# Optimization experiments

Hardware: AMD Instinct MI355X
Metric: run time of the kernel (lower is better)

## Reference

```python
import jax, jax.numpy as jnp
import numpy as np

B, S, D, P, H = 32, 1024, 512, 720, 4   # batch, seq_len (=codebook_size), enc_in, pred_len, heads
COMMIT_W, ORTHO_W = 1.0, 0.8


def setup_inputs() -> dict:
    key = jax.random.key(0)
    ks = jax.random.split(key, 6)
    return {
        "x": jax.random.normal(ks[0], (B, S, D), jnp.float32),
        "w_in": jax.random.normal(ks[1], (H * D, D), jnp.float32) * 0.02,   # project_in: dim -> heads*dim
        "b_in": jnp.zeros((H * D,), jnp.float32),
        "embed": jax.random.normal(ks[2], (H, S, D), jnp.float32),          # per-head codebook [h, C, d]
        "w_out": jax.random.normal(ks[3], (D, H * D), jnp.float32) * 0.02,  # project_out: heads*dim -> dim
        "b_out": jnp.zeros((D,), jnp.float32),
        "w_lin": jax.random.normal(ks[4], (P, S), jnp.float32) * 0.02,      # Linear over time axis
        "b_lin": jnp.zeros((P,), jnp.float32),
    }


def reference(x, w_in, b_in, embed, w_out, b_out, w_lin, b_lin):
    C = embed.shape[1]
    # Normalization: subtract last timestep (detached)
    seq_last = jax.lax.stop_gradient(x[:, -1:, :])          # [B,1,D]
    x0 = x - seq_last                                       # [B,S,D]

    # --- VectorQuantize ---
    xi = x0 @ w_in.T + b_in                                 # [B,S,H*D] project_in
    # 'b n (h d) -> h (b n) d' (separate codebook per head)
    f = xi.reshape(B, S, H, D).transpose(2, 0, 1, 3).reshape(H, B * S, D)
    # squared-euclidean distances to codes: [H, B*S, C]
    d2 = (jnp.sum(f * f, -1, keepdims=True)
          - 2.0 * jnp.einsum('hnd,hcd->hnc', f, embed)
          + jnp.sum(embed * embed, -1)[:, None, :])
    ind = jnp.argmin(d2, axis=-1)                           # [H, B*S]
    q = jnp.take_along_axis(embed, ind[:, :, None], axis=1)  # gather -> [H, B*S, D]

    # commitment loss (learnable codebook => quantize NOT detached)
    commit_loss = jnp.mean((q - f) ** 2)
    # orthogonal regularization on full codebook
    normed = embed / jnp.linalg.norm(embed, axis=-1, keepdims=True)
    cs = jnp.einsum('hid,hjd->hij', normed, normed)         # [H,C,C]
    ortho_loss = jnp.sum(cs ** 2) / (H * C * C) - 1.0 / C
    loss = COMMIT_W * commit_loss + ORTHO_W * ortho_loss

    # straight-through estimator
    q_st = f + jax.lax.stop_gradient(q - f)
    # 'h (b n) d -> b n (h d)'
    qo = q_st.reshape(H, B, S, D).transpose(1, 2, 0, 3).reshape(B, S, H * D)
    quantized = qo @ w_out.T + b_out                        # [B,S,D] project_out

    # Linear over the time axis: permute(0,2,1) -> Linear(S->P) -> permute back
    y = jnp.einsum('bnd,pn->bpd', quantized, w_lin) + b_lin[None, :, None]
    y = y + seq_last                                        # [B,P,D]

    indices = ind.reshape(H, B, S).transpose(1, 2, 0)       # [B,S,H]
    return y, indices, loss
```

## Files before the change

kernel.cpp:

```cpp
#include <hip/hip_runtime.h>
#include <stdint.h>

typedef unsigned int u32;
typedef unsigned long long u64;
typedef _Float16 f16;
typedef __attribute__((ext_vector_type(8))) _Float16 f16x8;
typedef __attribute__((ext_vector_type(4))) _Float16 f16x4;
typedef __attribute__((ext_vector_type(2))) _Float16 f16x2;
typedef __attribute__((ext_vector_type(4))) float f32x4;

#define MFMA16(a, b, c) __builtin_amdgcn_mfma_f32_16x16x32_f16((a), (b), (c), 0, 0, 0)
#define MARGIN 2.0f
#define WAITV(n) asm volatile("s_waitcnt vmcnt(" #n ")" ::: "memory")

__device__ __forceinline__ u32 ford(float x) { u32 u = __float_as_uint(x); return (u & 0x80000000u) ? ~u : (u | 0x80000000u); }
__device__ __forceinline__ float iford(u32 v) { u32 u = (v & 0x80000000u) ? (v & 0x7FFFFFFFu) : ~v; return __uint_as_float(u); }
__device__ __forceinline__ int xswz(int i, int n) { return (i & 7) * (n >> 3) + (i >> 3); }

typedef __attribute__((address_space(1))) const unsigned char ga_t;
typedef __attribute__((address_space(3))) unsigned char la_t;
__device__ __forceinline__ void gl16(const void* g, void* l) {
  __builtin_amdgcn_global_load_lds((ga_t*)g, (la_t*)l, 16, 0, 0);
}

__device__ __forceinline__ void stgp(const f16* g, int kt, char* sdst, int tid) {
#pragma unroll
  for (int it = 0; it < 2; ++it) {
    const int u = (tid + (it << 9)) << 4;
    const int r = u >> 7, sl = (u >> 4) & 7;
    const char* src = (const char*)g + (size_t)r * 1024 + ((size_t)kt << 7) +
                      (size_t)((sl ^ (r & 7)) << 4);
    gl16(src, sdst + u);
  }
}

__device__ __forceinline__ f16x8 rdf(const char* bb, int pb, int rr, int ks, int lane) {
  return *(const f16x8*)(bb + pb + rr * 128 +
                         ((((ks << 2) + (lane >> 4)) ^ (rr & 7)) << 4));
}

template <bool ISK1>
__global__ __launch_bounds__(512, 1) void gemm8(
    const f16* __restrict__ A0, const f16* __restrict__ A1,
    const f16* __restrict__ B0, const f16* __restrict__ B1,
    int chrows, void* __restrict__ out0, void* __restrict__ out1,
    const float* __restrict__ bias, const float* __restrict__ aux) {
  __shared__ char lds[131072 + (ISK1 ? 0 : 4096)];
  const int tid = threadIdx.x;
  const int lane = tid & 63, wid = tid >> 6;
  const int wm = wid >> 2, wn = wid & 3;

  int blkm, blkn, z = 0;
  {
    const int s = xswz(blockIdx.x, gridDim.x);
    if constexpr (ISK1) { blkn = s & 15; blkm = s >> 4; }
    else {
      const int bph = (chrows >> 8) << 2;
      z = s / bph;
      const int rem = s - z * bph;
      blkm = rem >> 2; blkn = rem & 3;
    }
  }

  if constexpr (!ISK1) {
    ((int*)(lds + 131072))[tid] = 0;
    ((int*)(lds + 131072))[tid + 512] = 0;
  }

  const f16 *p0, *p1, *p2, *p3;
  if constexpr (ISK1) {
    p0 = A0 + (size_t)blkm * 65536;
    p1 = A1 + (size_t)blkm * 65536;
    p2 = B0 + (size_t)blkn * 65536;
    p3 = B1 + (size_t)blkn * 65536;
  } else {
    p0 = A0 + ((size_t)z * chrows + (size_t)blkm * 256) * 512;
    p1 = p0 + 65536;
    p2 = B0 + (size_t)z * 524288 + (size_t)blkn * 131072;
    p3 = p2 + 65536;
  }

  constexpr int NACC = ISK1 ? 8 : 32;
  f32x4 acc[NACC];
#pragma unroll
  for (int i = 0; i < NACC; ++i) acc[i] = f32x4{0.f, 0.f, 0.f, 0.f};

  stgp(p0, 0, lds + 0, tid);
  stgp(p1, 0, lds + 16384, tid);
  stgp(p2, 0, lds + 32768, tid);
  stgp(p3, 0, lds + 49152, tid);

#pragma unroll
  for (int kc = 0; kc < 8; ++kc) {
    const char* bb = lds + (kc & 1) * 65536;
    char* nb = lds + ((kc + 1) & 1) * 65536;
    const bool pf = (kc + 1 < 8);
    WAITV(0);
    __builtin_amdgcn_s_barrier();

    if constexpr (!ISK1) {
      f16x8 a[4][2], b[4][2];
      const int pbA = wm * 16384;
      const int pbB = 32768 + (wn >> 1) * 16384;
      const int rB = (wn & 1) * 64 + (lane & 15);
#pragma unroll
      for (int mt = 0; mt < 4; ++mt)
#pragma unroll
        for (int ks = 0; ks < 2; ++ks) a[mt][ks] = rdf(bb, pbA, mt * 16 + (lane & 15), ks, lane);
#pragma unroll
      for (int nt = 0; nt < 2; ++nt)
#pragma unroll
        for (int ks = 0; ks < 2; ++ks) b[nt][ks] = rdf(bb, pbB, rB + nt * 16, ks, lane);
      if (pf) stgp(p0, kc + 1, nb + 0, tid);
      __builtin_amdgcn_s_setprio(1);
#pragma unroll
      for (int nt = 0; nt < 2; ++nt)
#pragma unroll
        for (int mt = 0; mt < 4; ++mt)
#pragma unroll
          for (int ks = 0; ks < 2; ++ks) acc[mt * 4 + nt] = MFMA16(a[mt][ks], b[nt][ks], acc[mt * 4 + nt]);
      __builtin_amdgcn_s_setprio(0);
#pragma unroll
      for (int nt = 2; nt < 4; ++nt)
#pragma unroll
        for (int ks = 0; ks < 2; ++ks) b[nt][ks] = rdf(bb, pbB, rB + nt * 16, ks, lane);
      if (pf) stgp(p1, kc + 1, nb + 16384, tid);
      __builtin_amdgcn_s_setprio(1);
#pragma unroll
      for (int nt = 2; nt < 4; ++nt)
#pragma unroll
        for (int mt = 0; mt < 4; ++mt)
#pragma unroll
          for (int ks = 0; ks < 2; ++ks) acc[mt * 4 + nt] = MFMA16(a[mt][ks], b[nt][ks], acc[mt * 4 + nt]);
      __builtin_amdgcn_s_setprio(0);
#pragma unroll
      for (int mt = 0; mt < 4; ++mt)
#pragma unroll
        for (int ks = 0; ks < 2; ++ks) a[mt][ks] = rdf(bb, pbA, (mt + 4) * 16 + (lane & 15), ks, lane);
      if (pf) stgp(p2, kc + 1, nb + 32768, tid);
      __builtin_amdgcn_s_setprio(1);
#pragma unroll
      for (int nt = 2; nt < 4; ++nt)
#pragma unroll
        for (int mt = 0; mt < 4; ++mt)
#pragma unroll
          for (int ks = 0; ks < 2; ++ks) acc[(mt + 4) * 4 + nt] = MFMA16(a[mt][ks], b[nt][ks], acc[(mt + 4) * 4 + nt]);
      __builtin_amdgcn_s_setprio(0);
      if (pf) stgp(p3, kc + 1, nb + 49152, tid);
      __builtin_amdgcn_s_setprio(1);
#pragma unroll
      for (int nt = 0; nt < 2; ++nt)
#pragma unroll
        for (int mt = 0; mt < 4; ++mt)
#pragma unroll
          for (int ks = 0; ks < 2; ++ks) acc[(mt + 4) * 4 + nt] = MFMA16(a[mt][ks], b[nt][ks], acc[(mt + 4) * 4 + nt]);
      __builtin_amdgcn_s_setprio(0);
    } else {
      f16x8 ah[2][2], al[2][2], bh[2][2], bl[2][2];
      const int rA = wm * 64 + (lane & 15);
      const int rB = wn * 32 + (lane & 15);
#pragma unroll
      for (int mt = 0; mt < 2; ++mt)
#pragma unroll
        for (int ks = 0; ks < 2; ++ks) {
          ah[mt][ks] = rdf(bb, 0, rA + mt * 16, ks, lane);
          al[mt][ks] = rdf(bb, 16384, rA + mt * 16, ks, lane);
        }
#pragma unroll
      for (int ks = 0; ks < 2; ++ks) {
        bh[0][ks] = rdf(bb, 32768, rB, ks, lane);
        bl[0][ks] = rdf(bb, 49152, rB, ks, lane);
      }
      if (pf) stgp(p0, kc + 1, nb + 0, tid);
      __builtin_amdgcn_s_setprio(1);
#pragma unroll
      for (int mt = 0; mt < 2; ++mt)
#pragma unroll
        for (int ks = 0; ks < 2; ++ks) {
          acc[mt * 2] = MFMA16(al[mt][ks], bh[0][ks], acc[mt * 2]);
          acc[mt * 2] = MFMA16(ah[mt][ks], bl[0][ks], acc[mt * 2]);
          acc[mt * 2] = MFMA16(ah[mt][ks], bh[0][ks], acc[mt * 2]);
        }
      __builtin_amdgcn_s_setprio(0);
#pragma unroll
      for (int ks = 0; ks < 2; ++ks) {
        bh[1][ks] = rdf(bb, 32768, rB + 16, ks, lane);
        bl[1][ks] = rdf(bb, 49152, rB + 16, ks, lane);
      }
      if (pf) stgp(p1, kc + 1, nb + 16384, tid);
      __builtin_amdgcn_s_setprio(1);
#pragma unroll
      for (int mt = 0; mt < 2; ++mt)
#pragma unroll
        for (int ks = 0; ks < 2; ++ks) {
          acc[mt * 2 + 1] = MFMA16(al[mt][ks], bh[1][ks], acc[mt * 2 + 1]);
          acc[mt * 2 + 1] = MFMA16(ah[mt][ks], bl[1][ks], acc[mt * 2 + 1]);
          acc[mt * 2 + 1] = MFMA16(ah[mt][ks], bh[1][ks], acc[mt * 2 + 1]);
        }
      __builtin_amdgcn_s_setprio(0);
#pragma unroll
      for (int mt = 0; mt < 2; ++mt)
#pragma unroll
        for (int ks = 0; ks < 2; ++ks) {
          ah[mt][ks] = rdf(bb, 0, rA + (mt + 2) * 16, ks, lane);
          al[mt][ks] = rdf(bb, 16384, rA + (mt + 2) * 16, ks, lane);
        }
      if (pf) stgp(p2, kc + 1, nb + 32768, tid);
      __builtin_amdgcn_s_setprio(1);
#pragma unroll
      for (int mt = 0; mt < 2; ++mt)
#pragma unroll
        for (int ks = 0; ks < 2; ++ks) {
          acc[(mt + 2) * 2 + 1] = MFMA16(al[mt][ks], bh[1][ks], acc[(mt + 2) * 2 + 1]);
          acc[(mt + 2) * 2 + 1] = MFMA16(ah[mt][ks], bl[1][ks], acc[(mt + 2) * 2 + 1]);
          acc[(mt + 2) * 2 + 1] = MFMA16(ah[mt][ks], bh[1][ks], acc[(mt + 2) * 2 + 1]);
        }
      __builtin_amdgcn_s_setprio(0);
      if (pf) stgp(p3, kc + 1, nb + 49152, tid);
      __builtin_amdgcn_s_setprio(1);
#pragma unroll
      for (int mt = 0; mt < 2; ++mt)
#pragma unroll
        for (int ks = 0; ks < 2; ++ks) {
          acc[(mt + 2) * 2] = MFMA16(al[mt][ks], bh[0][ks], acc[(mt + 2) * 2]);
          acc[(mt + 2) * 2] = MFMA16(ah[mt][ks], bl[0][ks], acc[(mt + 2) * 2]);
          acc[(mt + 2) * 2] = MFMA16(ah[mt][ks], bh[0][ks], acc[(mt + 2) * 2]);
        }
      __builtin_amdgcn_s_setprio(0);
    }
  }

  if constexpr (ISK1) {
    f16* fh = (f16*)out0;
    f16* fl = (f16*)out1;
#pragma unroll
    for (int nt = 0; nt < 2; ++nt) {
      const int gc = blkn * 128 + wn * 32 + nt * 16 + (lane & 15);
      const float bv = bias[gc];
      const int h = gc >> 9, d = gc & 511;
#pragma unroll
      for (int mt = 0; mt < 4; ++mt)
#pragma unroll
        for (int r = 0; r < 4; ++r) {
          const int grow = blkm * 128 + wm * 64 + mt * 16 + ((lane >> 4) << 2) + r;
          const float v = acc[mt * 2 + nt][r] * 6.103515625e-05f + bv;
          const f16 hv = (f16)v;
          const size_t off = ((size_t)h * chrows + grow) * 512 + d;
          fh[off] = hv;
          fl[off] = (f16)(v - (float)hv);
        }
    }
  } else {
    int* cntL = (int*)(lds + 131072);
    u64* candG = (u64*)out0;
    const int h = z;
    float escol[4];
    int cc[4];
#pragma unroll
    for (int nt = 0; nt < 4; ++nt) {
      cc[nt] = blkn * 256 + wn * 64 + nt * 16 + (lane & 15);
      escol[nt] = aux[h * 1024 + cc[nt]];
    }
#pragma unroll
    for (int mt = 0; mt < 8; ++mt)
#pragma unroll
      for (int r = 0; r < 4; ++r) {
        const int row_l = wm * 128 + mt * 16 + ((lane >> 4) << 2) + r;
        float vals[4];
        float mn = 3.4e38f;
#pragma unroll
        for (int nt = 0; nt < 4; ++nt) {
          const float v = escol[nt] - 2.0f * acc[mt * 4 + nt][r];
          vals[nt] = v;
          mn = fminf(mn, v);
        }
#pragma unroll
        for (int o = 1; o < 16; o <<= 1) mn = fminf(mn, __shfl_xor(mn, o));
        const float lim = mn + MARGIN;
#pragma unroll
        for (int nt = 0; nt < 4; ++nt)
          if (vals[nt] <= lim) {
            const int p = atomicAdd(&cntL[row_l * 4 + wn], 1);
            if (p < 4) {
              const size_t grow = (size_t)blkm * 256 + row_l;
              candG[((size_t)h * chrows + grow) * 64 + blkn * 16 + wn * 4 + p] =
                  ((u64)ford(vals[nt]) << 32) | (u32)cc[nt];
            }
          }
      }
  }
}

template <int LDK>
__device__ __forceinline__ void stg8k(const f16* gRowBase, int ktile, char* sdst, int tid) {
#pragma unroll
  for (int it = 0; it < 2; ++it) {
    const int u = (tid + (it << 8)) << 4;
    const int r = u >> 6, s = (u >> 4) & 3;
    const char* src = (const char*)gRowBase + (size_t)r * (LDK * 2) + ((size_t)ktile << 6) +
                      (size_t)((s ^ ((r >> 1) & 3)) << 4);
    gl16(src, sdst + u);
  }
}

template <int MODE>
__global__ __launch_bounds__(256, 3) void gemm2(
    const f16* __restrict__ Ah, const f16* __restrict__ Bh,
    void* __restrict__ out0, const float* __restrict__ bias,
    const float* __restrict__ aux, u64* __restrict__ slots) {
  constexpr int LDK = (MODE == 2 || MODE == 4) ? 1024 : 512;
  constexpr int D = 3;
  constexpr int KT = (MODE == 2 || MODE == 4) ? 32 : 16;
  constexpr int BUF = 16384;
  __shared__ char lds[D * BUF];

  const int tid = threadIdx.x;
  const int lane = tid & 63, wid = tid >> 6;
  const int wm = wid >> 1, wn = wid & 1;

  int blkm, blkn, z = 0;
  {
    const int s = xswz(blockIdx.x, gridDim.x);
    if constexpr (MODE == 1) { blkn = s & 3; blkm = s >> 2; z = blkm >> 3; }
    else if constexpr (MODE == 2) { blkn = s & 3; blkm = (s >> 2) & 3; z = s >> 4; }
    else { const int r2 = s % 24; blkm = r2 % 6; blkn = r2 / 6; z = s / 24; }
  }

  const f16 *Ab, *Bb;
  if constexpr (MODE == 1) {
    Ab = Ah + (size_t)blkm * 65536;
    Bb = Bh + (size_t)z * 262144 + (size_t)blkn * 65536;
  } else if constexpr (MODE == 2) {
    Ab = Ah + (size_t)z * 524288 + (size_t)blkm * 131072;
    Bb = Bh + (size_t)z * 524288 + (size_t)blkn * 131072;
  } else {
    Ab = Ah + (size_t)blkm * 131072;
    Bb = Bh + (size_t)z * 524288 + (size_t)blkn * 131072;
  }

  f32x4 acc[4][4];
#pragma unroll
  for (int i = 0; i < 4; ++i)
#pragma unroll
    for (int j = 0; j < 4; ++j) acc[i][j] = f32x4{0.f, 0.f, 0.f, 0.f};

  auto stage = [&](int kt, char* nb) {
    stg8k<LDK>(Ab, kt, nb, tid);
    stg8k<LDK>(Bb, kt, nb + 8192, tid);
  };
#pragma unroll
  for (int d = 0; d < D - 1; ++d) stage(d, lds + d * BUF);

#pragma unroll
  for (int kc = 0; kc < KT; ++kc) {
    if (kc + D - 1 < KT) stage(kc + D - 1, lds + ((kc + D - 1) % D) * BUF);
    const int nf = KT - 1 - kc;
    if (nf >= 2) WAITV(8);
    else if (nf == 1) WAITV(4);
    else WAITV(0);
    __builtin_amdgcn_s_barrier();
    const char* cbuf = lds + (kc % D) * BUF;
    f16x8 ah[4];
#pragma unroll
    for (int mt = 0; mt < 4; ++mt) {
      const int rr = wm * 64 + mt * 16 + (lane & 15);
      ah[mt] = *(const f16x8*)(cbuf + rr * 64 + (((lane >> 4) ^ ((rr >> 1) & 3)) << 4));
    }
    __builtin_amdgcn_s_setprio(1);
#pragma unroll
    for (int nt = 0; nt < 4; ++nt) {
      const int rn = wn * 64 + nt * 16 + (lane & 15);
      const f16x8 bh = *(const f16x8*)(cbuf + 8192 + rn * 64 + (((lane >> 4) ^ ((rn >> 1) & 3)) << 4));
#pragma unroll
      for (int mt = 0; mt < 4; ++mt) acc[mt][nt] = MFMA16(ah[mt], bh, acc[mt][nt]);
    }
    __builtin_amdgcn_s_setprio(0);
    __builtin_amdgcn_s_barrier();
  }

  if constexpr (MODE == 1) {
    f16* o = (f16*)out0;
#pragma unroll
    for (int nt = 0; nt < 4; ++nt) {
      const int gc = blkn * 128 + wn * 64 + nt * 16 + (lane & 15);
#pragma unroll
      for (int mt = 0; mt < 4; ++mt)
#pragma unroll
        for (int r = 0; r < 4; ++r) {
          const size_t grow = (size_t)blkm * 128 + wm * 64 + mt * 16 + ((lane >> 4) << 2) + r;
          o[grow * 512 + gc] = (f16)acc[mt][nt][r];
        }
    }
  } else if constexpr (MODE == 2) {
    float ssum = 0.f;
#pragma unroll
    for (int mt = 0; mt < 4; ++mt)
#pragma unroll
      for (int nt = 0; nt < 4; ++nt)
#pragma unroll
        for (int r = 0; r < 4; ++r) ssum += acc[mt][nt][r] * acc[mt][nt][r];
#pragma unroll
    for (int o = 1; o < 64; o <<= 1) ssum += __shfl_xor(ssum, o);
    float* wp = (float*)lds;
    __syncthreads();
    if (lane == 0) wp[wid] = ssum;
    __syncthreads();
    if (tid == 0) {
      const float p = wp[0] + wp[1] + wp[2] + wp[3];
      atomicAdd(slots + (blockIdx.x & 63), (u64)llrintf(p * 16777216.f));
    }
  } else {
    float* oy = (float*)out0 + (size_t)z * 368640;
    const float* xseq = aux + (size_t)z * 524288 + 523776;
    float sl[4];
    int gd[4];
#pragma unroll
    for (int nt = 0; nt < 4; ++nt) {
      gd[nt] = blkn * 128 + wn * 64 + nt * 16 + (lane & 15);
      sl[nt] = xseq[gd[nt]];
    }
#pragma unroll
    for (int mt = 0; mt < 4; ++mt)
#pragma unroll
      for (int r = 0; r < 4; ++r) {
        const int p = blkm * 128 + wm * 64 + mt * 16 + ((lane >> 4) << 2) + r;
        if (p < 720) {
          const float bp = bias[p];
#pragma unroll
          for (int nt = 0; nt < 4; ++nt) oy[(size_t)p * 512 + gd[nt]] = acc[mt][nt][r] + bp + sl[nt];
        }
      }
  }
}

__global__ __launch_bounds__(256, 4) void rescore_k(
    const u64* __restrict__ candG, const f16* __restrict__ fh,
    const f16* __restrict__ fl, const float* __restrict__ embed,
    int n0, int shCH,
    int* __restrict__ indw, float* __restrict__ indout, u64* __restrict__ cslots) {
  const int tid = threadIdx.x, lane = tid & 63, wid = tid >> 6;
  const int r = blockIdx.x * 4 + wid;
  const int h = r >> shCH, row = r & ((1 << shCH) - 1);
  u64 cu = candG[(size_t)r * 64 + lane];
  u64 mn = cu;
#pragma unroll
  for (int o = 1; o < 64; o <<= 1) { const u64 t = __shfl_xor(mn, o); if (t < mn) mn = t; }
  const float lim = iford((u32)(mn >> 32)) + MARGIN;
  const bool pass = iford((u32)(cu >> 32)) <= lim;
  u64 mask = __ballot(pass);
  float fv[8];
  {
    const size_t fo = (size_t)r * 512 + lane * 8;
    const f16x8 hv = *(const f16x8*)(fh + fo);
    const f16x8 lv = *(const f16x8*)(fl + fo);
#pragma unroll
    for (int j = 0; j < 8; ++j) fv[j] = (float)hv[j] + (float)lv[j];
  }
  double bestd = 1e300;
  int bestc = 0x7FFFFFFF;
  while (mask) {
    const int src = __ffsll((unsigned long long)mask) - 1;
    mask &= mask - 1;
    const int c = (int)(u32)__shfl(cu, src);
    const float* e = embed + ((size_t)h * 1024 + c) * 512 + lane * 8;
    const float4 e0 = *(const float4*)e, e1 = *(const float4*)(e + 4);
    const float ev[8] = {e0.x, e0.y, e0.z, e0.w, e1.x, e1.y, e1.z, e1.w};
    double sd = 0.0;
#pragma unroll
    for (int j = 0; j < 8; ++j) { const double d = (double)fv[j] - (double)ev[j]; sd += d * d; }
#pragma unroll
    for (int o = 1; o < 64; o <<= 1) sd += __shfl_xor(sd, o);
    if (sd < bestd || (sd == bestd && c < bestc)) { bestd = sd; bestc = c; }
  }
  if (lane == 0) {
    const int n = n0 + row;
    indw[(size_t)n * 4 + h] = bestc;
    indout[(size_t)n * 4 + h] = (float)bestc;
    atomicAdd(cslots + (blockIdx.x & 255), (u64)llrint(bestd * 65536.0));
  }
}

__global__ __launch_bounds__(256) void quantize_qT(
    const int* __restrict__ indw, const f16* __restrict__ Ep,
    const float* __restrict__ b_out, f16* __restrict__ qT) {
  const int tid = threadIdx.x;
  const int b = blockIdx.x >> 4, s0 = (blockIdx.x & 15) << 6;
  __shared__ int inds[64][4];
  inds[tid >> 2][tid & 3] = indw[(size_t)(b * 1024 + s0 + (tid >> 2)) * 4 + (tid & 3)];
  __syncthreads();
  const int d0 = tid * 2;
  const float ba0 = b_out[d0], ba1 = b_out[d0 + 1];
  u32 r0[32], r1[32];
  f16 t0 = (f16)0.f, t1 = (f16)0.f;
#pragma unroll
  for (int ss = 0; ss < 64; ++ss) {
    float a0 = ba0, a1 = ba1;
#pragma unroll
    for (int h = 0; h < 4; ++h) {
      const int c = inds[ss][h];
      const f16x2 p = *(const f16x2*)(Ep + (((size_t)h * 1024 + c) * 512 + d0));
      a0 += (float)p[0];
      a1 += (float)p[1];
    }
    const f16 q0 = (f16)a0, q1 = (f16)a1;
    if (ss & 1) {
      f16x2 w0; w0[0] = t0; w0[1] = q0; __builtin_memcpy(&r0[ss >> 1], &w0, 4);
      f16x2 w1; w1[0] = t1; w1[1] = q1; __builtin_memcpy(&r1[ss >> 1], &w1, 4);
    } else { t0 = q0; t1 = q1; }
  }
  const size_t o0 = ((size_t)b * 512 + d0) * 1024 + s0;
#pragma unroll
  for (int i = 0; i < 8; ++i) {
    uint4 v; v.x = r0[4 * i]; v.y = r0[4 * i + 1]; v.z = r0[4 * i + 2]; v.w = r0[4 * i + 3];
    *(uint4*)(qT + o0 + (size_t)i * 8) = v;
  }
  const size_t o1 = o0 + 1024;
#pragma unroll
  for (int i = 0; i < 8; ++i) {
    uint4 v; v.x = r1[4 * i]; v.y = r1[4 * i + 1]; v.z = r1[4 * i + 2]; v.w = r1[4 * i + 3];
    *(uint4*)(qT + o1 + (size_t)i * 8) = v;
  }
}

__global__ __launch_bounds__(256) void prep_x0(const float* __restrict__ x, int n0,
                                               f16* __restrict__ ht, f16* __restrict__ lt) {
  const int id = blockIdx.x * 256 + threadIdx.x;
  const int k8 = id & 63, r = id >> 6;
  const int n = n0 + r, b = n >> 10;
  const float* ap = x + (size_t)n * 512 + k8 * 8;
  const float* sp = x + (size_t)b * 524288 + 523776 + k8 * 8;
  const float4 a0 = *(const float4*)ap, a1 = *(const float4*)(ap + 4);
  const float4 s0 = *(const float4*)sp, s1 = *(const float4*)(sp + 4);
  const float v[8] = {(a0.x - s0.x) * 16.f, (a0.y - s0.y) * 16.f, (a0.z - s0.z) * 16.f,
                      (a0.w - s0.w) * 16.f, (a1.x - s1.x) * 16.f, (a1.y - s1.y) * 16.f,
                      (a1.z - s1.z) * 16.f, (a1.w - s1.w) * 16.f};
  f16x8 hv, lv;
#pragma unroll
  for (int j = 0; j < 8; ++j) { const f16 h = (f16)v[j]; hv[j] = h; lv[j] = (f16)(v[j] - (float)h); }
  const size_t off = (size_t)r * 512 + k8 * 8;
  *(f16x8*)(ht + off) = hv;
  *(f16x8*)(lt + off) = lv;
}

__global__ __launch_bounds__(256) void prep_win(const float* __restrict__ src,
                                                f16* __restrict__ hi, f16* __restrict__ lo) {
  const size_t e = ((size_t)blockIdx.x * 256 + threadIdx.x) * 4;
  const float4 v = *(const float4*)(src + e);
  const float w[4] = {v.x * 1024.f, v.y * 1024.f, v.z * 1024.f, v.w * 1024.f};
  f16x4 hv, lv;
#pragma unroll
  for (int j = 0; j < 4; ++j) { const f16 h = (f16)w[j]; hv[j] = h; lv[j] = (f16)(w[j] - (float)h); }
  *(f16x4*)(hi + e) = hv;
  *(f16x4*)(lo + e) = lv;
}

__global__ __launch_bounds__(256) void prep_embed_k(const float* __restrict__ em,
                                                    f16* __restrict__ ef,
                                                    float* __restrict__ esq,
                                                    float* __restrict__ invn) {
  const int tid = threadIdx.x, lane = tid & 63, wid = tid >> 6;
  const int row = blockIdx.x * 4 + wid;
  const float* er = em + (size_t)row * 512 + lane * 8;
  const float4 a = *(const float4*)er, b = *(const float4*)(er + 4);
  f16x8 v;
  v[0] = (f16)a.x; v[1] = (f16)a.y; v[2] = (f16)a.z; v[3] = (f16)a.w;
  v[4] = (f16)b.x; v[5] = (f16)b.y; v[6] = (f16)b.z; v[7] = (f16)b.w;
  *(f16x8*)(ef + (size_t)row * 512 + lane * 8) = v;
  float s = a.x * a.x + a.y * a.y + a.z * a.z + a.w * a.w +
            b.x * b.x + b.y * b.y + b.z * b.z + b.w * b.w;
#pragma unroll
  for (int o = 1; o < 64; o <<= 1) s += __shfl_xor(s, o);
  if (lane == 0) { esq[row] = s; invn[row] = 1.0f / sqrtf(s); }
}

__global__ __launch_bounds__(256) void prep_wout(const float* __restrict__ src,
                                                 f16* __restrict__ dst) {
  const int id = blockIdx.x * 256 + threadIdx.x;
  const int k8 = id & 63, rg = id >> 6;
  const int d = rg & 511, h = rg >> 9;
  const float* ap = src + (size_t)d * 2048 + h * 512 + k8 * 8;
  const float4 a0 = *(const float4*)ap, a1 = *(const float4*)(ap + 4);
  f16x8 v;
  v[0] = (f16)a0.x; v[1] = (f16)a0.y; v[2] = (f16)a0.z; v[3] = (f16)a0.w;
  v[4] = (f16)a1.x; v[5] = (f16)a1.y; v[6] = (f16)a1.z; v[7] = (f16)a1.w;
  *(f16x8*)(dst + (size_t)h * 262144 + (size_t)d * 512 + k8 * 8) = v;
}

__global__ __launch_bounds__(256) void prep_wlin(const float* __restrict__ src,
                                                 f16* __restrict__ dst) {
  const int id = blockIdx.x * 256 + threadIdx.x;
  const int k8 = id & 127, row = id >> 7;
  float4 a0 = {0.f, 0.f, 0.f, 0.f}, a1 = a0;
  if (row < 720) {
    const float* ap = src + (size_t)row * 1024 + k8 * 8;
    a0 = *(const float4*)ap;
    a1 = *(const float4*)(ap + 4);
  }
  f16x8 v;
  v[0] = (f16)a0.x; v[1] = (f16)a0.y; v[2] = (f16)a0.z; v[3] = (f16)a0.w;
  v[4] = (f16)a1.x; v[5] = (f16)a1.y; v[6] = (f16)a1.z; v[7] = (f16)a1.w;
  *(f16x8*)(dst + (size_t)row * 1024 + k8 * 8) = v;
}

__global__ __launch_bounds__(256) void prep_normT(const float* __restrict__ em,
                                                  const float* __restrict__ invn,
                                                  f16* __restrict__ nT) {
  __shared__ float t[64 * 65];
  const int tid = threadIdx.x;
  const int bx = blockIdx.x;
  const int h = bx >> 7, rem = bx & 127, cb = rem >> 3, db = rem & 7;
  const int c0 = cb * 64, d0 = db * 64;
  const int j = tid & 63, i0 = tid >> 6;
#pragma unroll
  for (int p = 0; p < 16; ++p) {
    const int i = p * 4 + i0;
    t[i * 65 + j] = em[(size_t)h * 524288 + (size_t)(c0 + i) * 512 + d0 + j] * invn[h * 1024 + c0 + i];
  }
  __syncthreads();
#pragma unroll
  for (int p = 0; p < 16; ++p) {
    const int i = p * 4 + i0;
    nT[(size_t)h * 524288 + (size_t)(d0 + i) * 1024 + c0 + j] = (f16)t[j * 65 + i];
  }
}

__global__ void finalize_k(const u64* __restrict__ cs, const u64* __restrict__ gs,
                           float* __restrict__ out) {
  const int lane = threadIdx.x;
  u64 c = cs[lane] + cs[lane + 64] + cs[lane + 128] + cs[lane + 192];
  u64 g = gs[lane];
#pragma unroll
  for (int o = 1; o < 64; o <<= 1) {
    c += __shfl_xor(c, o);
    g += __shfl_xor(g, o);
  }
  if (lane == 0) {
    const double commit = (double)c / 65536.0 / 67108864.0;
    const double ortho = (double)g / 16777216.0 / 4194304.0 - (1.0 / 1024.0);
    out[11927552] = (float)(commit + 0.8 * ortho);
  }
}

__global__ void ws_fail_k(float* out) {
  if (threadIdx.x == 0) out[11927552] = -777777.0f;
}

extern "C" void kernel_launch(void* const* d_in, const int* in_sizes, int n_in,
                              void* d_out, int out_size, void* d_ws, size_t ws_size,
                              hipStream_t stream) {
  (void)in_sizes; (void)n_in; (void)out_size;
  const float* x = (const float*)d_in[0];
  const float* w_in = (const float*)d_in[1];
  const float* b_in = (const float*)d_in[2];
  const float* embed = (const float*)d_in[3];
  const float* w_out = (const float*)d_in[4];
  const float* b_out = (const float*)d_in[5];
  const float* w_lin = (const float*)d_in[6];
  const float* b_lin = (const float*)d_in[7];
  float* out = (float*)d_out;
  char* ws = (char*)d_ws;

  constexpr size_t SZ_WIN = 2097152, SZ_EFT = 4194304, SZ_WOUT = 2097152;
  constexpr size_t SZ_EP = 4194304, SZ_WLIN = 1572864, SZ_NT = 4194304;
  constexpr size_t SZ_SMALL = 16384 + 16384 + 524288 + 2048 + 512;
  constexpr size_t FIXED = SZ_WIN * 2 + SZ_EFT + SZ_WOUT + SZ_EP + SZ_WLIN + SZ_NT + SZ_SMALL;

  int CH = 16384, shCH = 14;
  if (ws_size < FIXED + (size_t)16384 * 12288) { CH = 8192; shCH = 13; }
  if (ws_size < FIXED + (size_t)CH * 12288) {
    ws_fail_k<<<1, 64, 0, stream>>>(out);
    return;
  }

  size_t off = 0;
  f16* x0h = (f16*)(ws + off); off += (size_t)CH * 1024;
  f16* x0l = (f16*)(ws + off); off += (size_t)CH * 1024;
  f16* fh = (f16*)(ws + off); off += (size_t)CH * 4096;
  f16* fl = (f16*)(ws + off); off += (size_t)CH * 4096;
  u64* cand = (u64*)(ws + off); off += (size_t)CH * 2048;
  f16* winh = (f16*)(ws + off); off += SZ_WIN;
  f16* winl = (f16*)(ws + off); off += SZ_WIN;
  f16* eft = (f16*)(ws + off); off += SZ_EFT;
  f16* wout = (f16*)(ws + off); off += SZ_WOUT;
  f16* Ep = (f16*)(ws + off); off += SZ_EP;
  f16* wlint = (f16*)(ws + off); off += SZ_WLIN;
  f16* nT = (f16*)(ws + off); off += SZ_NT;
  float* esq = (float*)(ws + off); off += 16384;
  float* invn = (float*)(ws + off); off += 16384;
  int* indw = (int*)(ws + off); off += 524288;
  u64* cslots = (u64*)(ws + off); off += 2048;
  u64* gslots = (u64*)(ws + off); off += 512;
  f16* qT = (f16*)ws;

  hipMemsetAsync((void*)cslots, 0, 2560, stream);

  prep_win<<<1024, 256, 0, stream>>>(w_in, winh, winl);
  prep_embed_k<<<1024, 256, 0, stream>>>(embed, eft, esq, invn);
  prep_normT<<<512, 256, 0, stream>>>(embed, invn, nT);
  prep_wout<<<512, 256, 0, stream>>>(w_out, wout);
  prep_wlin<<<384, 256, 0, stream>>>(w_lin, wlint);

  gemm2<1><<<128, 256, 0, stream>>>(eft, wout, Ep, nullptr, nullptr, nullptr);
  gemm2<2><<<64, 256, 0, stream>>>(nT, nT, nullptr, nullptr, nullptr, gslots);

  for (int c0 = 0; c0 < 32768; c0 += CH) {
    prep_x0<<<CH / 4, 256, 0, stream>>>(x, c0, x0h, x0l);
    gemm8<true><<<(CH / 128) * 16, 512, 0, stream>>>(x0h, x0l, winh, winl, CH,
                                                     fh, fl, b_in, nullptr);
    hipMemsetAsync((void*)cand, 0xFF, (size_t)CH * 2048, stream);
    gemm8<false><<<(CH / 256) * 16, 512, 0, stream>>>(fh, nullptr, eft, nullptr, CH,
                                                      cand, nullptr, nullptr, esq);
    rescore_k<<<CH, 256, 0, stream>>>(cand, fh, fl, embed, c0, shCH,
                                      indw, out + 11796480, cslots);
  }

  quantize_qT<<<512, 256, 0, stream>>>(indw, Ep, b_out, qT);
  gemm2<4><<<768, 256, 0, stream>>>(wlint, qT, out, b_lin, x, nullptr);
  finalize_k<<<1, 64, 0, stream>>>(cslots, gslots, out);
}
```

Measured before the change: 697.5 us.

## Stage candidate lists in LDS, drop per-chunk memset, fuse prep kernels

```diff
diff --git a/kernel.cpp b/kernel.cpp
--- a/kernel.cpp
+++ b/kernel.cpp
@@ -251,7 +251,11 @@
         }
     }
   } else {
+    __syncthreads();
+    u64* candL = (u64*)lds;
     int* cntL = (int*)(lds + 131072);
+    for (int i = tid; i < 4096; i += 512) candL[i] = ~0ull;
+    __syncthreads();
     u64* candG = (u64*)out0;
     const int h = z;
     float escol[4];
@@ -281,13 +285,17 @@
         for (int nt = 0; nt < 4; ++nt)
           if (vals[nt] <= lim) {
             const int p = atomicAdd(&cntL[row_l * 4 + wn], 1);
-            if (p < 4) {
-              const size_t grow = (size_t)blkm * 256 + row_l;
-              candG[((size_t)h * chrows + grow) * 64 + blkn * 16 + wn * 4 + p] =
-                  ((u64)ford(vals[nt]) << 32) | (u32)cc[nt];
-            }
+            if (p < 4) candL[row_l * 16 + wn * 4 + p] = ((u64)ford(vals[nt]) << 32) | (u32)cc[nt];
           }
       }
+    __syncthreads();
+    if (tid < 256) {
+      const size_t grow = (size_t)blkm * 256 + tid;
+      u64* dst = candG + ((size_t)h * chrows + grow) * 64 + blkn * 16;
+      const u64* srcp = candL + tid * 16;
+#pragma unroll
+      for (int j = 0; j < 8; ++j) ((uint4*)dst)[j] = ((const uint4*)srcp)[j];
+    }
   }
 }
 
@@ -542,64 +550,60 @@
   *(f16x8*)(lt + off) = lv;
 }
 
-__global__ __launch_bounds__(256) void prep_win(const float* __restrict__ src,
-                                                f16* __restrict__ hi, f16* __restrict__ lo) {
-  const size_t e = ((size_t)blockIdx.x * 256 + threadIdx.x) * 4;
-  const float4 v = *(const float4*)(src + e);
-  const float w[4] = {v.x * 1024.f, v.y * 1024.f, v.z * 1024.f, v.w * 1024.f};
-  f16x4 hv, lv;
-#pragma unroll
-  for (int j = 0; j < 4; ++j) { const f16 h = (f16)w[j]; hv[j] = h; lv[j] = (f16)(w[j] - (float)h); }
-  *(f16x4*)(hi + e) = hv;
-  *(f16x4*)(lo + e) = lv;
-}
-
-__global__ __launch_bounds__(256) void prep_embed_k(const float* __restrict__ em,
-                                                    f16* __restrict__ ef,
-                                                    float* __restrict__ esq,
-                                                    float* __restrict__ invn) {
-  const int tid = threadIdx.x, lane = tid & 63, wid = tid >> 6;
-  const int row = blockIdx.x * 4 + wid;
-  const float* er = em + (size_t)row * 512 + lane * 8;
-  const float4 a = *(const float4*)er, b = *(const float4*)(er + 4);
-  f16x8 v;
-  v[0] = (f16)a.x; v[1] = (f16)a.y; v[2] = (f16)a.z; v[3] = (f16)a.w;
-  v[4] = (f16)b.x; v[5] = (f16)b.y; v[6] = (f16)b.z; v[7] = (f16)b.w;
-  *(f16x8*)(ef + (size_t)row * 512 + lane * 8) = v;
-  float s = a.x * a.x + a.y * a.y + a.z * a.z + a.w * a.w +
-            b.x * b.x + b.y * b.y + b.z * b.z + b.w * b.w;
-#pragma unroll
-  for (int o = 1; o < 64; o <<= 1) s += __shfl_xor(s, o);
-  if (lane == 0) { esq[row] = s; invn[row] = 1.0f / sqrtf(s); }
-}
-
-__global__ __launch_bounds__(256) void prep_wout(const float* __restrict__ src,
-                                                 f16* __restrict__ dst) {
-  const int id = blockIdx.x * 256 + threadIdx.x;
-  const int k8 = id & 63, rg = id >> 6;
-  const int d = rg & 511, h = rg >> 9;
-  const float* ap = src + (size_t)d * 2048 + h * 512 + k8 * 8;
-  const float4 a0 = *(const float4*)ap, a1 = *(const float4*)(ap + 4);
-  f16x8 v;
-  v[0] = (f16)a0.x; v[1] = (f16)a0.y; v[2] = (f16)a0.z; v[3] = (f16)a0.w;
-  v[4] = (f16)a1.x; v[5] = (f16)a1.y; v[6] = (f16)a1.z; v[7] = (f16)a1.w;
-  *(f16x8*)(dst + (size_t)h * 262144 + (size_t)d * 512 + k8 * 8) = v;
-}
-
-__global__ __launch_bounds__(256) void prep_wlin(const float* __restrict__ src,
-                                                 f16* __restrict__ dst) {
-  const int id = blockIdx.x * 256 + threadIdx.x;
-  const int k8 = id & 127, row = id >> 7;
-  float4 a0 = {0.f, 0.f, 0.f, 0.f}, a1 = a0;
-  if (row < 720) {
-    const float* ap = src + (size_t)row * 1024 + k8 * 8;
-    a0 = *(const float4*)ap;
-    a1 = *(const float4*)(ap + 4);
-  }
-  f16x8 v;
-  v[0] = (f16)a0.x; v[1] = (f16)a0.y; v[2] = (f16)a0.z; v[3] = (f16)a0.w;
-  v[4] = (f16)a1.x; v[5] = (f16)a1.y; v[6] = (f16)a1.z; v[7] = (f16)a1.w;
-  *(f16x8*)(dst + (size_t)row * 1024 + k8 * 8) = v;
+__global__ __launch_bounds__(256) void prep_all(
+    const float* __restrict__ w_in, f16* __restrict__ winh, f16* __restrict__ winl,
+    const float* __restrict__ em, f16* __restrict__ ef, float* __restrict__ esq,
+    float* __restrict__ invn, const float* __restrict__ w_out, f16* __restrict__ woutd,
+    const float* __restrict__ w_lin, f16* __restrict__ wlind) {
+  const int bx = blockIdx.x;
+  const int tid = threadIdx.x;
+  if (bx < 1024) {
+    const size_t e = ((size_t)bx * 256 + tid) * 4;
+    const float4 v = *(const float4*)(w_in + e);
+    const float w[4] = {v.x * 1024.f, v.y * 1024.f, v.z * 1024.f, v.w * 1024.f};
+    f16x4 hv, lv;
+#pragma unroll
+    for (int j = 0; j < 4; ++j) { const f16 h = (f16)w[j]; hv[j] = h; lv[j] = (f16)(w[j] - (float)h); }
+    *(f16x4*)(winh + e) = hv;
+    *(f16x4*)(winl + e) = lv;
+  } else if (bx < 2048) {
+    const int lane = tid & 63, wid = tid >> 6;
+    const int row = (bx - 1024) * 4 + wid;
+    const float* er = em + (size_t)row * 512 + lane * 8;
+    const float4 a = *(const float4*)er, b = *(const float4*)(er + 4);
+    f16x8 v;
+    v[0] = (f16)a.x; v[1] = (f16)a.y; v[2] = (f16)a.z; v[3] = (f16)a.w;
+    v[4] = (f16)b.x; v[5] = (f16)b.y; v[6] = (f16)b.z; v[7] = (f16)b.w;
+    *(f16x8*)(ef + (size_t)row * 512 + lane * 8) = v;
+    float s = a.x * a.x + a.y * a.y + a.z * a.z + a.w * a.w +
+              b.x * b.x + b.y * b.y + b.z * b.z + b.w * b.w;
+#pragma unroll
+    for (int o = 1; o < 64; o <<= 1) s += __shfl_xor(s, o);
+    if (lane == 0) { esq[row] = s; invn[row] = 1.0f / sqrtf(s); }
+  } else if (bx < 2560) {
+    const int id = (bx - 2048) * 256 + tid;
+    const int k8 = id & 63, rg = id >> 6;
+    const int d = rg & 511, h = rg >> 9;
+    const float* ap = w_out + (size_t)d * 2048 + h * 512 + k8 * 8;
+    const float4 a0 = *(const float4*)ap, a1 = *(const float4*)(ap + 4);
+    f16x8 v;
+    v[0] = (f16)a0.x; v[1] = (f16)a0.y; v[2] = (f16)a0.z; v[3] = (f16)a0.w;
+    v[4] = (f16)a1.x; v[5] = (f16)a1.y; v[6] = (f16)a1.z; v[7] = (f16)a1.w;
+    *(f16x8*)(woutd + (size_t)h * 262144 + (size_t)d * 512 + k8 * 8) = v;
+  } else {
+    const int id = (bx - 2560) * 256 + tid;
+    const int k8 = id & 127, row = id >> 7;
+    float4 a0 = {0.f, 0.f, 0.f, 0.f}, a1 = a0;
+    if (row < 720) {
+      const float* ap = w_lin + (size_t)row * 1024 + k8 * 8;
+      a0 = *(const float4*)ap;
+      a1 = *(const float4*)(ap + 4);
+    }
+    f16x8 v;
+    v[0] = (f16)a0.x; v[1] = (f16)a0.y; v[2] = (f16)a0.z; v[3] = (f16)a0.w;
+    v[4] = (f16)a1.x; v[5] = (f16)a1.y; v[6] = (f16)a1.z; v[7] = (f16)a1.w;
+    *(f16x8*)(wlind + (size_t)row * 1024 + k8 * 8) = v;
+  }
 }
 
 __global__ __launch_bounds__(256) void prep_normT(const float* __restrict__ em,
@@ -694,11 +698,9 @@
 
   hipMemsetAsync((void*)cslots, 0, 2560, stream);
 
-  prep_win<<<1024, 256, 0, stream>>>(w_in, winh, winl);
-  prep_embed_k<<<1024, 256, 0, stream>>>(embed, eft, esq, invn);
+  prep_all<<<2944, 256, 0, stream>>>(w_in, winh, winl, embed, eft, esq, invn,
+                                     w_out, wout, w_lin, wlint);
   prep_normT<<<512, 256, 0, stream>>>(embed, invn, nT);
-  prep_wout<<<512, 256, 0, stream>>>(w_out, wout);
-  prep_wlin<<<384, 256, 0, stream>>>(w_lin, wlint);
 
   gemm2<1><<<128, 256, 0, stream>>>(eft, wout, Ep, nullptr, nullptr, nullptr);
   gemm2<2><<<64, 256, 0, stream>>>(nT, nT, nullptr, nullptr, nullptr, gslots);
@@ -707,7 +709,6 @@
     prep_x0<<<CH / 4, 256, 0, stream>>>(x, c0, x0h, x0l);
     gemm8<true><<<(CH / 128) * 16, 512, 0, stream>>>(x0h, x0l, winh, winl, CH,
                                                      fh, fl, b_in, nullptr);
-    hipMemsetAsync((void*)cand, 0xFF, (size_t)CH * 2048, stream);
     gemm8<false><<<(CH / 256) * 16, 512, 0, stream>>>(fh, nullptr, eft, nullptr, CH,
                                                       cand, nullptr, nullptr, esq);
     rescore_k<<<CH, 256, 0, stream>>>(cand, fh, fl, embed, c0, shCH,
```

Measured after the change: 695.9 us. No clear change (-0.2%).
